# Optimization experiments

Measured on AMD Instinct MI355X. Metric: run time of the kernel, lower is better.

The kernel has to match this reference:

```python
import jax, jax.numpy as jnp
import numpy as np
import math

B, C, N, L = 32, 128, 2048, 1
H, DK, APT = 8, 16, 10
EPS = 1e-5


def conv1x1(x, W, b):
    # 1x1 Conv2d on [B, C, N, L]
    return jnp.einsum('oc,bcnl->bonl', W, x) + b[None, :, None, None]


def layer_norm_12(x):
    # normalize over dims (1, 2) as in the custom LayerNorm (no affine)
    mean = x.mean(axis=(1, 2), keepdims=True)
    var = x.var(axis=(1, 2), keepdims=True)
    return (x - mean) / jnp.sqrt(var + EPS)


def setup_inputs() -> dict:
    key = jax.random.key(0)
    ks = jax.random.split(key, 10)
    s = 0.05  # small-scale init for numerical stability
    inp = {
        'input': jax.random.normal(ks[0], (B, C, N, L), jnp.float32),
        'Wq': jax.random.normal(ks[1], (C, C), jnp.float32) * s,
        'bq': jnp.zeros((C,), jnp.float32),
        'Wv': jax.random.normal(ks[2], (C, C), jnp.float32) * s,
        'bv': jnp.zeros((C,), jnp.float32),
        'Wc': jax.random.normal(ks[3], (C, C), jnp.float32) * s,
        'bc': jnp.zeros((C,), jnp.float32),
        'memory': jax.random.normal(ks[4], (H, L, N, DK), jnp.float32) * s,
        'sa_weight': jnp.ones((C, N, L), jnp.float32),
        'sa_bias': jnp.zeros((C, N, L), jnp.float32),
        'nodevec1': jax.random.normal(ks[5], (N, APT), jnp.float32),
        'nodevec2': jax.random.normal(ks[6], (APT, N), jnp.float32),
        'Wg1': jax.random.normal(ks[7], (C, C), jnp.float32) * s,
        'bg1': jnp.zeros((C,), jnp.float32),
        'Wg2': jax.random.normal(ks[8], (C, C), jnp.float32) * s,
        'bg2': jnp.zeros((C,), jnp.float32),
        'Wg3': jax.random.normal(ks[9], (C, C), jnp.float32) * s,
        'bg3': jnp.zeros((C,), jnp.float32),
    }
    return inp


def reference(input, Wq, bq, Wv, bv, Wc, bc, memory, sa_weight, sa_bias,
              nodevec1, nodevec2, Wg1, bg1, Wg2, bg2, Wg3, bg3):
    scale = math.sqrt(DK)

    def split_heads(t):  # [B,C,N,L] -> [B,H,L,N,DK]
        return t.reshape(B, H, DK, N, L).transpose(0, 1, 4, 3, 2)

    # SpatialAttention (Conv = 1x1 conv + relu; dropout off in eval)
    q = jax.nn.relu(conv1x1(input, Wq, bq))
    v = jax.nn.relu(conv1x1(input, Wv, bv))
    query = jax.nn.softmax(split_heads(q) / scale, axis=-1)     # [B,H,L,N,DK]
    value = split_heads(v)                                       # [B,H,L,N,DK]
    key = jax.nn.softmax(memory / scale, axis=-1)                # [H,L,N,DK]
    Aapt = jax.nn.softmax(jax.nn.relu(nodevec1 @ nodevec2), axis=-1)  # [N,N]

    kv = jnp.einsum('hlnx,bhlny->bhlxy', key, value)             # [B,H,L,DK,DK]
    attn_qkv = jnp.einsum('bhlnx,bhlxy->bhlny', query, kv)       # [B,H,L,N,DK]
    attn_dyn = jnp.einsum('nm,bhlnc->bhlnc', Aapt, value)        # row-sum scaling
    x = attn_qkv + attn_dyn

    # merge heads back to [B,C,N,L] and apply concat conv (Conv = conv+relu)
    x = x.transpose(0, 1, 4, 3, 2).reshape(B, C, N, L)
    x = jax.nn.relu(conv1x1(x, Wc, bc))
    x = x * sa_weight[None] + sa_bias[None] + x                  # affine branch

    # Encoder wrap
    x = x + input
    x = layer_norm_12(x)
    g = conv1x1(x, Wg1, bg1) * jax.nn.sigmoid(conv1x1(x, Wg2, bg2))
    g = conv1x1(g, Wg3, bg3)                                     # GLU
    x = g + x
    x = x * sa_weight[None] + sa_bias[None] + x
    x = layer_norm_12(x)
    return x
```

## Files before the change

kernel.cpp:

```cpp
#include <hip/hip_runtime.h>
#include <hip/hip_bf16.h>
#include <math.h>

#define DI __device__ __forceinline__

typedef short bf16x8 __attribute__((ext_vector_type(8)));
typedef float f32x4 __attribute__((ext_vector_type(4)));

constexpr int BB = 32, CC = 128, NN = 2048;
constexpr float EPSf = 1e-5f;
constexpr float RCN = 1.0f / (CC * (float)NN);

#define MFMA(a,b,c) __builtin_amdgcn_mfma_f32_16x16x32_bf16(a,b,c,0,0,0)

DI unsigned short f2b(float f){
    union { __hip_bfloat16 h; unsigned short u; } v;
    v.h = __float2bfloat16(f);
    return v.u;
}
DI float b2f(unsigned short h){
    union { unsigned u; float f; } v; v.u = ((unsigned)h) << 16;
    return v.f;
}
DI float sigm(float x){ return 1.0f / (1.0f + __expf(-x)); }

__global__ __launch_bounds__(256) void k_prep(
    const float* __restrict__ Wq, const float* __restrict__ Wv,
    const float* __restrict__ Wc, const float* __restrict__ Wg1,
    const float* __restrict__ Wg2, const float* __restrict__ Wg3,
    const float* __restrict__ mem, const float* __restrict__ saw,
    const float* __restrict__ sab,
    unsigned short* __restrict__ Wb, float* __restrict__ rs,
    unsigned short* __restrict__ ksT, unsigned short* __restrict__ sawb,
    unsigned short* __restrict__ sabb)
{
    const int tid = threadIdx.x;
    if (blockIdx.x < 96) {
        const int i = blockIdx.x * 256 + tid;
        const int m = i >> 12, q = i & 4095;
        const float* src = (m==0)?Wq:(m==1)?Wv:(m==2)?Wc:(m==3)?Wg1:(m==4)?Wg2:Wg3;
        f32x4 w = *(const f32x4*)&src[q * 4];
        ushort4 p; p.x=f2b(w[0]); p.y=f2b(w[1]); p.z=f2b(w[2]); p.w=f2b(w[3]);
        *(ushort4*)&Wb[(size_t)m * 16384 + q * 4] = p;
    } else if (blockIdx.x == 96) {
        const float* src = (tid < 128) ? Wg1 : Wg2;
        const int o = tid & 127;
        float s = 0.f;
#pragma unroll
        for (int j = 0; j < 32; j++) {
            f32x4 a = *(const f32x4*)&src[o * 128 + j * 4];
            s += a[0] + a[1] + a[2] + a[3];
        }
        rs[tid] = s;
    } else if (blockIdx.x < 161) {
        const int row = (blockIdx.x - 97) * 256 + tid;
        const int h = row >> 11, n = row & 2047;
        const float* p = mem + (size_t)row * 16;
        float v[16];
        f32x4 t0 = *(const f32x4*)(p);
        f32x4 t1 = *(const f32x4*)(p + 4);
        f32x4 t2 = *(const f32x4*)(p + 8);
        f32x4 t3 = *(const f32x4*)(p + 12);
#pragma unroll
        for (int j = 0; j < 4; j++) { v[j]=t0[j]; v[4+j]=t1[j]; v[8+j]=t2[j]; v[12+j]=t3[j]; }
        float mx = v[0];
#pragma unroll
        for (int x = 1; x < 16; x++) mx = fmaxf(mx, v[x]);
        float s = 0.f;
#pragma unroll
        for (int x = 0; x < 16; x++) { v[x] = __expf((v[x] - mx) * 0.25f); s += v[x]; }
        const float is = 1.0f / s;
#pragma unroll
        for (int x = 0; x < 16; x++)
            ksT[((size_t)(h * 16 + x)) * NN + n] = f2b(v[x] * is);
    } else {
        const int i = (blockIdx.x - 161) * 256 + tid;
        const int m = i >> 16, q = i & 65535;
        const float* src = m ? sab : saw;
        unsigned short* dst = m ? sabb : sawb;
        f32x4 w = *(const f32x4*)&src[q * 4];
        ushort4 p; p.x=f2b(w[0]); p.y=f2b(w[1]); p.z=f2b(w[2]); p.w=f2b(w[3]);
        *(ushort4*)&dst[q * 4] = p;
    }
}

__global__ __launch_bounds__(256,1) void k_qv(
    const float* __restrict__ in, const unsigned short* __restrict__ WqB,
    const unsigned short* __restrict__ WvB, const float* __restrict__ bq,
    const float* __restrict__ bv, unsigned short* __restrict__ qT,
    unsigned short* __restrict__ vT, unsigned short* __restrict__ inT)
{
    __shared__ unsigned short tile[128 * 136];
    const int b = blockIdx.x >> 4, n0 = (blockIdx.x & 15) * 128;
    const int tid = threadIdx.x, l = tid & 63, wid = tid >> 6;
    const int wo = wid & 1, wn = wid >> 1, lr = l & 15, lg = l >> 4;
    f32x4 accq[4][4], accv[4][4];
    const f32x4 z = {0.f,0.f,0.f,0.f};
#pragma unroll
    for (int i = 0; i < 4; i++)
#pragma unroll
        for (int j = 0; j < 4; j++) { accq[i][j] = z; accv[i][j] = z; }
    const float* inb = in + (size_t)b * CC * NN;
#pragma unroll
    for (int ks = 0; ks < 4; ks++) {
        const int cb = ks * 32 + lg * 8;
        bf16x8 aq[4], av[4];
#pragma unroll
        for (int mf = 0; mf < 4; mf++) {
            const int o = wo*64 + mf*16 + lr;
            aq[mf] = *(const bf16x8*)&WqB[o * 128 + cb];
            av[mf] = *(const bf16x8*)&WvB[o * 128 + cb];
        }
        bf16x8 bx[4];
#pragma unroll
        for (int nf = 0; nf < 4; nf++) {
            const int n = n0 + wn*64 + nf*16 + lr;
            union { bf16x8 v; unsigned short u[8]; } t;
#pragma unroll
            for (int j = 0; j < 8; j++) t.u[j] = f2b(inb[(size_t)(cb + j) * NN + n]);
            bx[nf] = t.v;
        }
        if (wo == 0) {
#pragma unroll
            for (int nf = 0; nf < 4; nf++)
                *(bf16x8*)&tile[(wn*64 + nf*16 + lr) * 136 + cb] = bx[nf];
        }
#pragma unroll
        for (int mf = 0; mf < 4; mf++)
#pragma unroll
            for (int nf = 0; nf < 4; nf++) {
                accq[mf][nf] = MFMA(aq[mf], bx[nf], accq[mf][nf]);
                accv[mf][nf] = MFMA(av[mf], bx[nf], accv[mf][nf]);
            }
    }
    __syncthreads();
#pragma unroll
    for (int p = 0; p < 8; p++) {
        const int row = p*16 + (tid >> 4), col = (tid & 15) * 8;
        *(uint4*)&inT[((size_t)b * NN + n0 + row) * CC + col] =
            *(const uint4*)&tile[row * 136 + col];
    }
    __syncthreads();
#pragma unroll
    for (int mf = 0; mf < 4; mf++) {
        const int ob = wo*64 + mf*16 + lg*4;
        const f32x4 b4 = *(const f32x4*)&bq[ob];
#pragma unroll
        for (int nf = 0; nf < 4; nf++) {
            const int nl = wn*64 + nf*16 + lr;
            f32x4 a = accq[mf][nf];
            ushort4 pk;
            pk.x = f2b(fmaxf(a[0]+b4[0],0.f)); pk.y = f2b(fmaxf(a[1]+b4[1],0.f));
            pk.z = f2b(fmaxf(a[2]+b4[2],0.f)); pk.w = f2b(fmaxf(a[3]+b4[3],0.f));
            *(ushort4*)&tile[nl * 136 + ob] = pk;
        }
    }
    __syncthreads();
#pragma unroll
    for (int p = 0; p < 8; p++) {
        const int row = p*16 + (tid >> 4), col = (tid & 15) * 8;
        *(uint4*)&qT[((size_t)b * NN + n0 + row) * CC + col] =
            *(const uint4*)&tile[row * 136 + col];
    }
    __syncthreads();
#pragma unroll
    for (int mf = 0; mf < 4; mf++) {
        const int ob = wo*64 + mf*16 + lg*4;
        const f32x4 b4 = *(const f32x4*)&bv[ob];
#pragma unroll
        for (int nf = 0; nf < 4; nf++) {
            const int nl = wn*64 + nf*16 + lr;
            f32x4 a = accv[mf][nf];
            ushort4 pk;
            pk.x = f2b(fmaxf(a[0]+b4[0],0.f)); pk.y = f2b(fmaxf(a[1]+b4[1],0.f));
            pk.z = f2b(fmaxf(a[2]+b4[2],0.f)); pk.w = f2b(fmaxf(a[3]+b4[3],0.f));
            *(ushort4*)&tile[nl * 136 + ob] = pk;
        }
    }
    __syncthreads();
#pragma unroll
    for (int p = 0; p < 8; p++) {
        const int row = p*16 + (tid >> 4), col = (tid & 15) * 8;
        *(uint4*)&vT[((size_t)b * NN + n0 + row) * CC + col] =
            *(const uint4*)&tile[row * 136 + col];
    }
}

__global__ __launch_bounds__(256) void k_kv(const unsigned short* __restrict__ ksT,
                                            const unsigned short* __restrict__ vT,
                                            float* __restrict__ kvb)
{
    __shared__ unsigned short vt[4 * 16 * 520];
    __shared__ float red[1024];
    const int b = blockIdx.x >> 3, h = blockIdx.x & 7;
    const int tid = threadIdx.x, l = tid & 63, wid = tid >> 6;
    const int n0 = wid * 512;
    unsigned short* vtw = vt + wid * (16 * 520);
    const unsigned short* vb = vT + ((size_t)b * NN + n0) * CC + h * 16;
#pragma unroll
    for (int r = 0; r < 8; r++) {
        const int nl = r * 64 + l;
        uint4 q0 = *(const uint4*)&vb[(size_t)nl * CC];
        uint4 q1 = *(const uint4*)&vb[(size_t)nl * CC + 8];
        const unsigned uu[8] = {q0.x,q0.y,q0.z,q0.w,q1.x,q1.y,q1.z,q1.w};
#pragma unroll
        for (int k = 0; k < 8; k++) {
            vtw[(2*k)*520 + nl]   = (unsigned short)(uu[k] & 0xffffu);
            vtw[(2*k+1)*520 + nl] = (unsigned short)(uu[k] >> 16);
        }
    }
    const int lr = l & 15, lg = l >> 4;
    const unsigned short* ka = ksT + (size_t)h * 16 * NN;
    f32x4 acc = {0.f,0.f,0.f,0.f};
#pragma unroll
    for (int kk = 0; kk < 16; kk++) {
        bf16x8 af = *(const bf16x8*)&ka[(size_t)lr * NN + n0 + kk*32 + lg*8];
        bf16x8 bf = *(const bf16x8*)&vtw[lr * 520 + kk*32 + lg*8];
        acc = MFMA(af, bf, acc);
    }
#pragma unroll
    for (int r = 0; r < 4; r++)
        red[wid * 256 + (lg*4 + r) * 16 + lr] = acc[r];
    __syncthreads();
    {
        const float s = red[tid] + red[256 + tid] + red[512 + tid] + red[768 + tid];
        kvb[((size_t)(b * 8 + h)) * 256 + tid] = s;
    }
}

__global__ __launch_bounds__(256,2) void k_attnC(
    const unsigned short* __restrict__ qT, unsigned short* __restrict__ vT,
    const float* __restrict__ kvb, const unsigned short* __restrict__ WcB,
    const float* __restrict__ bc, const unsigned short* __restrict__ sawb,
    const unsigned short* __restrict__ sabb, const unsigned short* __restrict__ inT,
    float* __restrict__ part1)
{
    __shared__ float kvl[8 * 260];
    __shared__ unsigned short xc[128 * 136];
    __shared__ float red[8];
    const int b = blockIdx.x >> 4, n0 = (blockIdx.x & 15) * 128;
    const int tid = threadIdx.x;
    {
        const float* kp = kvb + (size_t)b * 2048 + (tid >> 5) * 256 + (tid & 31) * 8;
        f32x4 v0 = *(const f32x4*)kp;
        f32x4 v1 = *(const f32x4*)(kp + 4);
        float* dst = &kvl[(tid >> 5) * 260 + (tid & 31) * 8];
        *(f32x4*)dst = v0; *(f32x4*)(dst + 4) = v1;
    }
    __syncthreads();
#pragma unroll 1
    for (int it = 0; it < 4; it++) {
        const int idx = it * 256 + tid;
        const int nl = idx >> 3, h = idx & 7;
        const size_t base = ((size_t)b * NN + n0 + nl) * CC + h * 16;
        uint4 u0 = *(const uint4*)(qT + base);
        uint4 u1 = *(const uint4*)(qT + base + 8);
        uint4 w0 = *(const uint4*)(vT + base);
        uint4 w1 = *(const uint4*)(vT + base + 8);
        unsigned uu[8] = {u0.x,u0.y,u0.z,u0.w,u1.x,u1.y,u1.z,u1.w};
        float mx = -1e30f;
#pragma unroll
        for (int j = 0; j < 8; j++) {
            mx = fmaxf(mx, b2f((unsigned short)(uu[j] & 0xffffu)));
            mx = fmaxf(mx, b2f((unsigned short)(uu[j] >> 16)));
        }
        const float* kh = &kvl[h * 260];
        f32x4 r0 = {0,0,0,0}, r1 = {0,0,0,0}, r2 = {0,0,0,0}, r3 = {0,0,0,0};
        float s = 0.f;
#pragma unroll
        for (int x = 0; x < 16; x++) {
            const unsigned short qh = (x & 1) ? (unsigned short)(uu[x >> 1] >> 16)
                                              : (unsigned short)(uu[x >> 1] & 0xffffu);
            const float e = __expf((b2f(qh) - mx) * 0.25f);
            s += e;
            const f32x4 k0 = *(const f32x4*)&kh[x * 16];
            const f32x4 k1 = *(const f32x4*)&kh[x * 16 + 4];
            const f32x4 k2 = *(const f32x4*)&kh[x * 16 + 8];
            const f32x4 k3 = *(const f32x4*)&kh[x * 16 + 12];
#pragma unroll
            for (int j = 0; j < 4; j++) {
                r0[j] = fmaf(e, k0[j], r0[j]);
                r1[j] = fmaf(e, k1[j], r1[j]);
                r2[j] = fmaf(e, k2[j], r2[j]);
                r3[j] = fmaf(e, k3[j], r3[j]);
            }
        }
        const float is = 1.0f / s;
        unsigned vv[8] = {w0.x,w0.y,w0.z,w0.w,w1.x,w1.y,w1.z,w1.w};
        unsigned short* xp = &xc[nl * 136 + h * 16];
#pragma unroll
        for (int j2 = 0; j2 < 4; j2++) {
            const f32x4 rr = (j2==0)?r0:(j2==1)?r1:(j2==2)?r2:r3;
            ushort4 pk;
            pk.x = f2b(rr[0]*is + b2f((unsigned short)(vv[2*j2]   & 0xffffu)));
            pk.y = f2b(rr[1]*is + b2f((unsigned short)(vv[2*j2]   >> 16)));
            pk.z = f2b(rr[2]*is + b2f((unsigned short)(vv[2*j2+1] & 0xffffu)));
            pk.w = f2b(rr[3]*is + b2f((unsigned short)(vv[2*j2+1] >> 16)));
            *(ushort4*)&xp[j2 * 4] = pk;
        }
    }
    __syncthreads();
    const int l = tid & 63, wid = tid >> 6;
    const int wo = wid & 1, wn = wid >> 1, lr = l & 15, lg = l >> 4;
    f32x4 acc[4][4];
    const f32x4 z = {0.f,0.f,0.f,0.f};
#pragma unroll
    for (int i = 0; i < 4; i++)
#pragma unroll
        for (int j = 0; j < 4; j++) acc[i][j] = z;
#pragma unroll
    for (int ks = 0; ks < 4; ks++) {
        const int cb = ks * 32 + lg * 8;
        bf16x8 af[4];
#pragma unroll
        for (int mf = 0; mf < 4; mf++)
            af[mf] = *(const bf16x8*)&WcB[(wo*64 + mf*16 + lr) * 128 + cb];
        bf16x8 bx[4];
#pragma unroll
        for (int nf = 0; nf < 4; nf++)
            bx[nf] = *(const bf16x8*)&xc[(wn*64 + nf*16 + lr) * 136 + cb];
#pragma unroll
        for (int mf = 0; mf < 4; mf++)
#pragma unroll
            for (int nf = 0; nf < 4; nf++)
                acc[mf][nf] = MFMA(af[mf], bx[nf], acc[mf][nf]);
    }
    __syncthreads();
    float sum = 0.f, ssq = 0.f;
#pragma unroll
    for (int mf = 0; mf < 4; mf++) {
        const int ob = wo*64 + mf*16 + lg*4;
        const f32x4 b4 = *(const f32x4*)&bc[ob];
#pragma unroll
        for (int nf = 0; nf < 4; nf++) {
            const int nl = wn*64 + nf*16 + lr;
            const int n = n0 + nl;
            f32x4 a = acc[mf][nf];
            const ushort4 iu = *(const ushort4*)&inT[((size_t)b * NN + n) * CC + ob];
            float ys[4];
#pragma unroll
            for (int r = 0; r < 4; r++) {
                const int o = ob + r;
                const float t = fmaxf(a[r] + b4[r], 0.f);
                const float sw = b2f(sawb[(size_t)o * NN + n]);
                const float sb = b2f(sabb[(size_t)o * NN + n]);
                const unsigned short iv = (r==0)?iu.x:(r==1)?iu.y:(r==2)?iu.z:iu.w;
                float y = t * sw + sb + t + b2f(iv);
                sum += y; ssq += y * y;
                ys[r] = y;
            }
            ushort4 pk;
            pk.x = f2b(ys[0]); pk.y = f2b(ys[1]); pk.z = f2b(ys[2]); pk.w = f2b(ys[3]);
            *(ushort4*)&xc[nl * 136 + ob] = pk;
        }
        __builtin_amdgcn_sched_barrier(0);
    }
    __syncthreads();
#pragma unroll
    for (int p = 0; p < 8; p++) {
        const int row = p*16 + (tid >> 4), col = (tid & 15) * 8;
        *(uint4*)&vT[((size_t)b * NN + n0 + row) * CC + col] =
            *(const uint4*)&xc[row * 136 + col];
    }
#pragma unroll
    for (int off = 32; off > 0; off >>= 1) {
        sum += __shfl_down(sum, off);
        ssq += __shfl_down(ssq, off);
    }
    if ((tid & 63) == 0) { red[wid*2] = sum; red[wid*2+1] = ssq; }
    __syncthreads();
    if (tid == 0) {
        part1[2 * blockIdx.x]     = red[0]+red[2]+red[4]+red[6];
        part1[2 * blockIdx.x + 1] = red[1]+red[3]+red[5]+red[7];
    }
}

__global__ __launch_bounds__(256,1) void k_glu3(
    const unsigned short* __restrict__ y1,
    const unsigned short* __restrict__ W1B, const unsigned short* __restrict__ W2B,
    const unsigned short* __restrict__ W3B,
    const float* __restrict__ b1, const float* __restrict__ b2,
    const float* __restrict__ b3, const float* __restrict__ rs,
    const float* __restrict__ part1, const unsigned short* __restrict__ sawb,
    const unsigned short* __restrict__ sabb, unsigned short* __restrict__ X2,
    float* __restrict__ part2)
{
    __shared__ unsigned short yt[128 * 136];
    __shared__ unsigned short gx[128 * 136];
    __shared__ float cs[256];
    __shared__ float red[8];
    const int b = blockIdx.x >> 4, n0 = (blockIdx.x & 15) * 128;
    const int tid = threadIdx.x;
    float s0 = 0.f, q0 = 0.f;
#pragma unroll
    for (int t = 0; t < 16; t++) { s0 += part1[(b*16+t)*2]; q0 += part1[(b*16+t)*2+1]; }
    const float mean = s0 * RCN;
    const float var  = q0 * RCN - mean * mean;
    const float inv  = rsqrtf(var + EPSf);
    {
        const int cq = tid & 15;
#pragma unroll
        for (int it = 0; it < 8; it++) {
            const int n = it * 16 + (tid >> 4);
            uint4 u = *(const uint4*)&y1[((size_t)b * NN + n0 + n) * CC + cq * 8];
            *(uint4*)&yt[n * 136 + cq * 8] = u;
        }
    }
    {
        const int o = tid & 127;
        const float bb = (tid < 128) ? b1[o] : b2[o];
        cs[tid] = bb - mean * inv * rs[tid];
    }
    __syncthreads();
    const int l = tid & 63, wid = tid >> 6;
    const int wo = wid & 1, wn = wid >> 1, lr = l & 15, lg = l >> 4;
    {
        f32x4 acc1[4][4], acc2[4][4];
        const f32x4 z = {0.f,0.f,0.f,0.f};
#pragma unroll
        for (int i = 0; i < 4; i++)
#pragma unroll
            for (int j = 0; j < 4; j++) { acc1[i][j] = z; acc2[i][j] = z; }
#pragma unroll
        for (int ks = 0; ks < 4; ks++) {
            const int cb = ks * 32 + lg * 8;
            bf16x8 a1[4], a2[4];
#pragma unroll
            for (int mf = 0; mf < 4; mf++) {
                const int o = wo*64 + mf*16 + lr;
                a1[mf] = *(const bf16x8*)&W1B[o * 128 + cb];
                a2[mf] = *(const bf16x8*)&W2B[o * 128 + cb];
            }
            bf16x8 bx[4];
#pragma unroll
            for (int nf = 0; nf < 4; nf++)
                bx[nf] = *(const bf16x8*)&yt[(wn*64 + nf*16 + lr) * 136 + cb];
#pragma unroll
            for (int mf = 0; mf < 4; mf++)
#pragma unroll
                for (int nf = 0; nf < 4; nf++) {
                    acc1[mf][nf] = MFMA(a1[mf], bx[nf], acc1[mf][nf]);
                    acc2[mf][nf] = MFMA(a2[mf], bx[nf], acc2[mf][nf]);
                }
        }
#pragma unroll
        for (int mf = 0; mf < 4; mf++) {
            const int ob = wo*64 + mf*16 + lg*4;
            const f32x4 c1 = *(const f32x4*)&cs[ob];
            const f32x4 c2 = *(const f32x4*)&cs[128 + ob];
#pragma unroll
            for (int nf = 0; nf < 4; nf++) {
                const int nl = wn*64 + nf*16 + lr;
                ushort4 pk;
                float g1, g2;
                g1 = acc1[mf][nf][0]*inv + c1[0]; g2 = acc2[mf][nf][0]*inv + c2[0];
                pk.x = f2b(g1 * sigm(g2));
                g1 = acc1[mf][nf][1]*inv + c1[1]; g2 = acc2[mf][nf][1]*inv + c2[1];
                pk.y = f2b(g1 * sigm(g2));
                g1 = acc1[mf][nf][2]*inv + c1[2]; g2 = acc2[mf][nf][2]*inv + c2[2];
                pk.z = f2b(g1 * sigm(g2));
                g1 = acc1[mf][nf][3]*inv + c1[3]; g2 = acc2[mf][nf][3]*inv + c2[3];
                pk.w = f2b(g1 * sigm(g2));
                *(ushort4*)&gx[nl * 136 + ob] = pk;
            }
        }
    }
    __syncthreads();
    f32x4 acc[4][4];
    const f32x4 z = {0.f,0.f,0.f,0.f};
#pragma unroll
    for (int i = 0; i < 4; i++)
#pragma unroll
        for (int j = 0; j < 4; j++) acc[i][j] = z;
#pragma unroll
    for (int ks = 0; ks < 4; ks++) {
        const int cb = ks * 32 + lg * 8;
        bf16x8 af[4];
#pragma unroll
        for (int mf = 0; mf < 4; mf++)
            af[mf] = *(const bf16x8*)&W3B[(wo*64 + mf*16 + lr) * 128 + cb];
        bf16x8 bx[4];
#pragma unroll
        for (int nf = 0; nf < 4; nf++)
            bx[nf] = *(const bf16x8*)&gx[(wn*64 + nf*16 + lr) * 136 + cb];
#pragma unroll
        for (int mf = 0; mf < 4; mf++)
#pragma unroll
            for (int nf = 0; nf < 4; nf++)
                acc[mf][nf] = MFMA(af[mf], bx[nf], acc[mf][nf]);
    }
    __syncthreads();
    float sum = 0.f, ssq = 0.f;
#pragma unroll
    for (int mf = 0; mf < 4; mf++) {
        const int ob = wo*64 + mf*16 + lg*4;
        const f32x4 b4 = *(const f32x4*)&b3[ob];
#pragma unroll
        for (int nf = 0; nf < 4; nf++) {
            const int nl = wn*64 + nf*16 + lr;
            const int n = n0 + nl;
            ushort4 yq = *(const ushort4*)&yt[nl * 136 + ob];
            f32x4 a = acc[mf][nf];
            float ys[4];
#pragma unroll
            for (int r = 0; r < 4; r++) {
                const int o = ob + r;
                const unsigned short ev = (r==0)?yq.x:(r==1)?yq.y:(r==2)?yq.z:yq.w;
                const float t = a[r] + b4[r] + (b2f(ev) - mean) * inv;
                const float sw = b2f(sawb[(size_t)o * NN + n]);
                const float sb = b2f(sabb[(size_t)o * NN + n]);
                const float y = t * sw + sb + t;
                sum += y; ssq += y * y;
                ys[r] = y;
            }
            ushort4 pk;
            pk.x = f2b(ys[0]); pk.y = f2b(ys[1]); pk.z = f2b(ys[2]); pk.w = f2b(ys[3]);
            *(ushort4*)&gx[nl * 136 + ob] = pk;
        }
        __builtin_amdgcn_sched_barrier(0);
    }
    __syncthreads();
#pragma unroll
    for (int p = 0; p < 8; p++) {
        const int row = p*16 + (tid >> 4), col = (tid & 15) * 8;
        *(uint4*)&X2[((size_t)b * NN + n0 + row) * CC + col] =
            *(const uint4*)&gx[row * 136 + col];
    }
#pragma unroll
    for (int off = 32; off > 0; off >>= 1) {
        sum += __shfl_down(sum, off);
        ssq += __shfl_down(ssq, off);
    }
    if ((tid & 63) == 0) { red[wid*2] = sum; red[wid*2+1] = ssq; }
    __syncthreads();
    if (tid == 0) {
        part2[2 * blockIdx.x]     = red[0]+red[2]+red[4]+red[6];
        part2[2 * blockIdx.x + 1] = red[1]+red[3]+red[5]+red[7];
    }
}

__global__ __launch_bounds__(256) void k_lnfin(const unsigned short* __restrict__ x2,
                                               const float* __restrict__ part2,
                                               float* __restrict__ out)
{
    __shared__ unsigned ts[64 * 69];
    const int b = blockIdx.x >> 5, n0 = (blockIdx.x & 31) * 64;
    const int tid = threadIdx.x;
    float s0 = 0.f, q0 = 0.f;
#pragma unroll
    for (int t = 0; t < 16; t++) { s0 += part2[(b*16+t)*2]; q0 += part2[(b*16+t)*2+1]; }
    const float mean = s0 * RCN;
    const float var  = q0 * RCN - mean * mean;
    const float inv  = rsqrtf(var + EPSf);
    {
        const int n = tid >> 2, qd = tid & 3;
        const unsigned short* src = x2 + ((size_t)b * NN + n0 + n) * CC + qd * 32;
        uint4 a0 = *(const uint4*)(src);
        uint4 a1 = *(const uint4*)(src + 8);
        uint4 a2 = *(const uint4*)(src + 16);
        uint4 a3 = *(const uint4*)(src + 24);
        unsigned u[16] = {a0.x,a0.y,a0.z,a0.w, a1.x,a1.y,a1.z,a1.w,
                          a2.x,a2.y,a2.z,a2.w, a3.x,a3.y,a3.z,a3.w};
#pragma unroll
        for (int k = 0; k < 16; k++)
            ts[(qd * 16 + k) * 69 + n] = u[k];
    }
    __syncthreads();
#pragma unroll
    for (int pass = 0; pass < 8; pass++) {
        const int c = pass * 16 + (tid >> 4), nq = tid & 15;
        const int cp = c >> 1, hi = c & 1;
        f32x4 v;
#pragma unroll
        for (int j = 0; j < 4; j++) {
            const unsigned u = ts[cp * 69 + nq * 4 + j];
            const unsigned short hv = hi ? (unsigned short)(u >> 16)
                                         : (unsigned short)(u & 0xffffu);
            v[j] = (b2f(hv) - mean) * inv;
        }
        *(f32x4*)&out[((size_t)b * CC + c) * NN + n0 + nq * 4] = v;
    }
}

extern "C" void kernel_launch(void* const* d_in, const int* in_sizes, int n_in,
                              void* d_out, int out_size, void* d_ws, size_t ws_size,
                              hipStream_t stream)
{
    const float* input = (const float*)d_in[0];
    const float* Wq  = (const float*)d_in[1];
    const float* bq  = (const float*)d_in[2];
    const float* Wv  = (const float*)d_in[3];
    const float* bv  = (const float*)d_in[4];
    const float* Wc  = (const float*)d_in[5];
    const float* bc  = (const float*)d_in[6];
    const float* mem = (const float*)d_in[7];
    const float* saw = (const float*)d_in[8];
    const float* sab = (const float*)d_in[9];
    const float* Wg1 = (const float*)d_in[12];
    const float* bg1 = (const float*)d_in[13];
    const float* Wg2 = (const float*)d_in[14];
    const float* bg2 = (const float*)d_in[15];
    const float* Wg3 = (const float*)d_in[16];
    const float* bg3 = (const float*)d_in[17];
    float* out = (float*)d_out;

    unsigned char* wsb = (unsigned char*)d_ws;
    unsigned short* qT  = (unsigned short*)(wsb);
    unsigned short* vT  = (unsigned short*)(wsb + 16777216);
    unsigned short* ksT = (unsigned short*)(wsb + 33554432);
    float* kvb   = (float*)(wsb + 34078720);
    unsigned short* Wb  = (unsigned short*)(wsb + 34340864);
    float* rs    = (float*)(wsb + 34537472);
    float* part1 = (float*)(wsb + 34538496);
    float* part2 = (float*)(wsb + 34542592);
    unsigned short* inT  = (unsigned short*)d_out;
    unsigned short* sawb = (unsigned short*)((unsigned char*)d_out + 16777216);
    unsigned short* sabb = sawb + 262144;

    k_prep <<<673,  256, 0, stream>>>(Wq, Wv, Wc, Wg1, Wg2, Wg3, mem, saw, sab,
                                      Wb, rs, ksT, sawb, sabb);
    k_qv   <<<512,  256, 0, stream>>>(input, Wb, Wb + 16384, bq, bv, qT, vT, inT);
    k_kv   <<<256,  256, 0, stream>>>(ksT, vT, kvb);
    k_attnC<<<512,  256, 0, stream>>>(qT, vT, kvb, Wb + 2*16384, bc, sawb, sabb,
                                      inT, part1);
    k_glu3 <<<512,  256, 0, stream>>>(vT, Wb + 3*16384, Wb + 4*16384, Wb + 5*16384,
                                      bg1, bg2, bg3, rs, part1, sawb, sabb, qT, part2);
    k_lnfin<<<1024, 256, 0, stream>>>(qT, part2, out);
}
```

Baseline: 124.9 us.

## Move Q projection into attention kernel and split dual GEMMs to raise occupancy

Measured after the change: 119.7 us. -4.1%, faster.

```diff
diff --git a/kernel.cpp b/kernel.cpp
--- a/kernel.cpp
+++ b/kernel.cpp
@@ -84,33 +84,29 @@
     }
 }
 
-__global__ __launch_bounds__(256,1) void k_qv(
-    const float* __restrict__ in, const unsigned short* __restrict__ WqB,
-    const unsigned short* __restrict__ WvB, const float* __restrict__ bq,
-    const float* __restrict__ bv, unsigned short* __restrict__ qT,
-    unsigned short* __restrict__ vT, unsigned short* __restrict__ inT)
+__global__ __launch_bounds__(256,2) void k_v(
+    const float* __restrict__ in, const unsigned short* __restrict__ WvB,
+    const float* __restrict__ bv, unsigned short* __restrict__ vT,
+    unsigned short* __restrict__ inT)
 {
     __shared__ unsigned short tile[128 * 136];
     const int b = blockIdx.x >> 4, n0 = (blockIdx.x & 15) * 128;
     const int tid = threadIdx.x, l = tid & 63, wid = tid >> 6;
     const int wo = wid & 1, wn = wid >> 1, lr = l & 15, lg = l >> 4;
-    f32x4 accq[4][4], accv[4][4];
+    f32x4 acc[4][4];
     const f32x4 z = {0.f,0.f,0.f,0.f};
 #pragma unroll
     for (int i = 0; i < 4; i++)
 #pragma unroll
-        for (int j = 0; j < 4; j++) { accq[i][j] = z; accv[i][j] = z; }
+        for (int j = 0; j < 4; j++) acc[i][j] = z;
     const float* inb = in + (size_t)b * CC * NN;
 #pragma unroll
     for (int ks = 0; ks < 4; ks++) {
         const int cb = ks * 32 + lg * 8;
-        bf16x8 aq[4], av[4];
-#pragma unroll
-        for (int mf = 0; mf < 4; mf++) {
-            const int o = wo*64 + mf*16 + lr;
-            aq[mf] = *(const bf16x8*)&WqB[o * 128 + cb];
-            av[mf] = *(const bf16x8*)&WvB[o * 128 + cb];
-        }
+        bf16x8 av[4];
+#pragma unroll
+        for (int mf = 0; mf < 4; mf++)
+            av[mf] = *(const bf16x8*)&WvB[(wo*64 + mf*16 + lr) * 128 + cb];
         bf16x8 bx[4];
 #pragma unroll
         for (int nf = 0; nf < 4; nf++) {
@@ -128,10 +124,8 @@
 #pragma unroll
         for (int mf = 0; mf < 4; mf++)
 #pragma unroll
-            for (int nf = 0; nf < 4; nf++) {
-                accq[mf][nf] = MFMA(aq[mf], bx[nf], accq[mf][nf]);
-                accv[mf][nf] = MFMA(av[mf], bx[nf], accv[mf][nf]);
-            }
+            for (int nf = 0; nf < 4; nf++)
+                acc[mf][nf] = MFMA(av[mf], bx[nf], acc[mf][nf]);
     }
     __syncthreads();
 #pragma unroll
@@ -144,33 +138,11 @@
 #pragma unroll
     for (int mf = 0; mf < 4; mf++) {
         const int ob = wo*64 + mf*16 + lg*4;
-        const f32x4 b4 = *(const f32x4*)&bq[ob];
+        const f32x4 b4 = *(const f32x4*)&bv[ob];
 #pragma unroll
         for (int nf = 0; nf < 4; nf++) {
             const int nl = wn*64 + nf*16 + lr;
-            f32x4 a = accq[mf][nf];
-            ushort4 pk;
-            pk.x = f2b(fmaxf(a[0]+b4[0],0.f)); pk.y = f2b(fmaxf(a[1]+b4[1],0.f));
-            pk.z = f2b(fmaxf(a[2]+b4[2],0.f)); pk.w = f2b(fmaxf(a[3]+b4[3],0.f));
-            *(ushort4*)&tile[nl * 136 + ob] = pk;
-        }
-    }
-    __syncthreads();
-#pragma unroll
-    for (int p = 0; p < 8; p++) {
-        const int row = p*16 + (tid >> 4), col = (tid & 15) * 8;
-        *(uint4*)&qT[((size_t)b * NN + n0 + row) * CC + col] =
-            *(const uint4*)&tile[row * 136 + col];
-    }
-    __syncthreads();
-#pragma unroll
-    for (int mf = 0; mf < 4; mf++) {
-        const int ob = wo*64 + mf*16 + lg*4;
-        const f32x4 b4 = *(const f32x4*)&bv[ob];
-#pragma unroll
-        for (int nf = 0; nf < 4; nf++) {
-            const int nl = wn*64 + nf*16 + lr;
-            f32x4 a = accv[mf][nf];
+            f32x4 a = acc[mf][nf];
             ushort4 pk;
             pk.x = f2b(fmaxf(a[0]+b4[0],0.f)); pk.y = f2b(fmaxf(a[1]+b4[1],0.f));
             pk.z = f2b(fmaxf(a[2]+b4[2],0.f)); pk.w = f2b(fmaxf(a[3]+b4[3],0.f));
@@ -229,14 +201,15 @@
 }
 
 __global__ __launch_bounds__(256,2) void k_attnC(
-    const unsigned short* __restrict__ qT, unsigned short* __restrict__ vT,
-    const float* __restrict__ kvb, const unsigned short* __restrict__ WcB,
-    const float* __restrict__ bc, const unsigned short* __restrict__ sawb,
-    const unsigned short* __restrict__ sabb, const unsigned short* __restrict__ inT,
+    const unsigned short* __restrict__ inT, unsigned short* __restrict__ vT,
+    const float* __restrict__ kvb,
+    const unsigned short* __restrict__ WqB, const float* __restrict__ bq,
+    const unsigned short* __restrict__ WcB, const float* __restrict__ bc,
+    const unsigned short* __restrict__ sawb, const unsigned short* __restrict__ sabb,
     float* __restrict__ part1)
 {
     __shared__ float kvl[8 * 260];
-    __shared__ unsigned short xc[128 * 136];
+    __shared__ unsigned short xq[128 * 136];
     __shared__ float red[8];
     const int b = blockIdx.x >> 4, n0 = (blockIdx.x & 15) * 128;
     const int tid = threadIdx.x;
@@ -247,16 +220,59 @@
         float* dst = &kvl[(tid >> 5) * 260 + (tid & 31) * 8];
         *(f32x4*)dst = v0; *(f32x4*)(dst + 4) = v1;
     }
+    const int l = tid & 63, wid = tid >> 6;
+    const int wo = wid & 1, wn = wid >> 1, lr = l & 15, lg = l >> 4;
+    {
+        f32x4 acc[4][4];
+        const f32x4 z = {0.f,0.f,0.f,0.f};
+#pragma unroll
+        for (int i = 0; i < 4; i++)
+#pragma unroll
+            for (int j = 0; j < 4; j++) acc[i][j] = z;
+        const unsigned short* ab = inT + (size_t)b * NN * CC;
+#pragma unroll
+        for (int ks = 0; ks < 4; ks++) {
+            const int cb = ks * 32 + lg * 8;
+            bf16x8 af[4];
+#pragma unroll
+            for (int mf = 0; mf < 4; mf++)
+                af[mf] = *(const bf16x8*)&WqB[(wo*64 + mf*16 + lr) * 128 + cb];
+            bf16x8 bx[4];
+#pragma unroll
+            for (int nf = 0; nf < 4; nf++)
+                bx[nf] = *(const bf16x8*)&ab[(size_t)(n0 + wn*64 + nf*16 + lr) * CC + cb];
+#pragma unroll
+            for (int mf = 0; mf < 4; mf++)
+#pragma unroll
+                for (int nf = 0; nf < 4; nf++)
+                    acc[mf][nf] = MFMA(af[mf], bx[nf], acc[mf][nf]);
+        }
+#pragma unroll
+        for (int mf = 0; mf < 4; mf++) {
+            const int ob = wo*64 + mf*16 + lg*4;
+            const f32x4 b4 = *(const f32x4*)&bq[ob];
+#pragma unroll
+            for (int nf = 0; nf < 4; nf++) {
+                const int nl = wn*64 + nf*16 + lr;
+                f32x4 a = acc[mf][nf];
+                ushort4 pk;
+                pk.x = f2b(fmaxf(a[0]+b4[0],0.f)); pk.y = f2b(fmaxf(a[1]+b4[1],0.f));
+                pk.z = f2b(fmaxf(a[2]+b4[2],0.f)); pk.w = f2b(fmaxf(a[3]+b4[3],0.f));
+                *(ushort4*)&xq[nl * 136 + ob] = pk;
+            }
+        }
+    }
     __syncthreads();
 #pragma unroll 1
     for (int it = 0; it < 4; it++) {
         const int idx = it * 256 + tid;
         const int nl = idx >> 3, h = idx & 7;
         const size_t base = ((size_t)b * NN + n0 + nl) * CC + h * 16;
-        uint4 u0 = *(const uint4*)(qT + base);
-        uint4 u1 = *(const uint4*)(qT + base + 8);
         uint4 w0 = *(const uint4*)(vT + base);
         uint4 w1 = *(const uint4*)(vT + base + 8);
+        const unsigned short* qp = &xq[nl * 136 + h * 16];
+        uint4 u0 = *(const uint4*)qp;
+        uint4 u1 = *(const uint4*)(qp + 8);
         unsigned uu[8] = {u0.x,u0.y,u0.z,u0.w,u1.x,u1.y,u1.z,u1.w};
         float mx = -1e30f;
 #pragma unroll
@@ -287,7 +303,7 @@
         }
         const float is = 1.0f / s;
         unsigned vv[8] = {w0.x,w0.y,w0.z,w0.w,w1.x,w1.y,w1.z,w1.w};
-        unsigned short* xp = &xc[nl * 136 + h * 16];
+        unsigned short* xp = &xq[nl * 136 + h * 16];
 #pragma unroll
         for (int j2 = 0; j2 < 4; j2++) {
             const f32x4 rr = (j2==0)?r0:(j2==1)?r1:(j2==2)?r2:r3;
@@ -300,8 +316,6 @@
         }
     }
     __syncthreads();
-    const int l = tid & 63, wid = tid >> 6;
-    const int wo = wid & 1, wn = wid >> 1, lr = l & 15, lg = l >> 4;
     f32x4 acc[4][4];
     const f32x4 z = {0.f,0.f,0.f,0.f};
 #pragma unroll
@@ -318,7 +332,7 @@
         bf16x8 bx[4];
 #pragma unroll
         for (int nf = 0; nf < 4; nf++)
-            bx[nf] = *(const bf16x8*)&xc[(wn*64 + nf*16 + lr) * 136 + cb];
+            bx[nf] = *(const bf16x8*)&xq[(wn*64 + nf*16 + lr) * 136 + cb];
 #pragma unroll
         for (int mf = 0; mf < 4; mf++)
 #pragma unroll
@@ -351,16 +365,15 @@
             }
             ushort4 pk;
             pk.x = f2b(ys[0]); pk.y = f2b(ys[1]); pk.z = f2b(ys[2]); pk.w = f2b(ys[3]);
-            *(ushort4*)&xc[nl * 136 + ob] = pk;
-        }
-        __builtin_amdgcn_sched_barrier(0);
+            *(ushort4*)&xq[nl * 136 + ob] = pk;
+        }
     }
     __syncthreads();
 #pragma unroll
     for (int p = 0; p < 8; p++) {
         const int row = p*16 + (tid >> 4), col = (tid & 15) * 8;
         *(uint4*)&vT[((size_t)b * NN + n0 + row) * CC + col] =
-            *(const uint4*)&xc[row * 136 + col];
+            *(const uint4*)&xq[row * 136 + col];
     }
 #pragma unroll
     for (int off = 32; off > 0; off >>= 1) {
@@ -375,7 +388,7 @@
     }
 }
 
-__global__ __launch_bounds__(256,1) void k_glu3(
+__global__ __launch_bounds__(256,2) void k_glu3(
     const unsigned short* __restrict__ y1,
     const unsigned short* __restrict__ W1B, const unsigned short* __restrict__ W2B,
     const unsigned short* __restrict__ W3B,
@@ -414,23 +427,20 @@
     __syncthreads();
     const int l = tid & 63, wid = tid >> 6;
     const int wo = wid & 1, wn = wid >> 1, lr = l & 15, lg = l >> 4;
-    {
-        f32x4 acc1[4][4], acc2[4][4];
-        const f32x4 z = {0.f,0.f,0.f,0.f};
+    const f32x4 z = {0.f,0.f,0.f,0.f};
+    {
+        f32x4 acc[4][4];
 #pragma unroll
         for (int i = 0; i < 4; i++)
 #pragma unroll
-            for (int j = 0; j < 4; j++) { acc1[i][j] = z; acc2[i][j] = z; }
+            for (int j = 0; j < 4; j++) acc[i][j] = z;
 #pragma unroll
         for (int ks = 0; ks < 4; ks++) {
             const int cb = ks * 32 + lg * 8;
-            bf16x8 a1[4], a2[4];
-#pragma unroll
-            for (int mf = 0; mf < 4; mf++) {
-                const int o = wo*64 + mf*16 + lr;
-                a1[mf] = *(const bf16x8*)&W1B[o * 128 + cb];
-                a2[mf] = *(const bf16x8*)&W2B[o * 128 + cb];
-            }
+            bf16x8 af[4];
+#pragma unroll
+            for (int mf = 0; mf < 4; mf++)
+                af[mf] = *(const bf16x8*)&W1B[(wo*64 + mf*16 + lr) * 128 + cb];
             bf16x8 bx[4];
 #pragma unroll
             for (int nf = 0; nf < 4; nf++)
@@ -438,36 +448,67 @@
 #pragma unroll
             for (int mf = 0; mf < 4; mf++)
 #pragma unroll
-                for (int nf = 0; nf < 4; nf++) {
-                    acc1[mf][nf] = MFMA(a1[mf], bx[nf], acc1[mf][nf]);
-                    acc2[mf][nf] = MFMA(a2[mf], bx[nf], acc2[mf][nf]);
-                }
+                for (int nf = 0; nf < 4; nf++)
+                    acc[mf][nf] = MFMA(af[mf], bx[nf], acc[mf][nf]);
         }
 #pragma unroll
         for (int mf = 0; mf < 4; mf++) {
             const int ob = wo*64 + mf*16 + lg*4;
             const f32x4 c1 = *(const f32x4*)&cs[ob];
-            const f32x4 c2 = *(const f32x4*)&cs[128 + ob];
 #pragma unroll
             for (int nf = 0; nf < 4; nf++) {
                 const int nl = wn*64 + nf*16 + lr;
+                f32x4 a = acc[mf][nf];
                 ushort4 pk;
-                float g1, g2;
-                g1 = acc1[mf][nf][0]*inv + c1[0]; g2 = acc2[mf][nf][0]*inv + c2[0];
-                pk.x = f2b(g1 * sigm(g2));
-                g1 = acc1[mf][nf][1]*inv + c1[1]; g2 = acc2[mf][nf][1]*inv + c2[1];
-                pk.y = f2b(g1 * sigm(g2));
-                g1 = acc1[mf][nf][2]*inv + c1[2]; g2 = acc2[mf][nf][2]*inv + c2[2];
-                pk.z = f2b(g1 * sigm(g2));
-                g1 = acc1[mf][nf][3]*inv + c1[3]; g2 = acc2[mf][nf][3]*inv + c2[3];
-                pk.w = f2b(g1 * sigm(g2));
+                pk.x = f2b(a[0]*inv + c1[0]); pk.y = f2b(a[1]*inv + c1[1]);
+                pk.z = f2b(a[2]*inv + c1[2]); pk.w = f2b(a[3]*inv + c1[3]);
                 *(ushort4*)&gx[nl * 136 + ob] = pk;
             }
         }
     }
+    {
+        f32x4 acc[4][4];
+#pragma unroll
+        for (int i = 0; i < 4; i++)
+#pragma unroll
+            for (int j = 0; j < 4; j++) acc[i][j] = z;
+#pragma unroll
+        for (int ks = 0; ks < 4; ks++) {
+            const int cb = ks * 32 + lg * 8;
+            bf16x8 af[4];
+#pragma unroll
+            for (int mf = 0; mf < 4; mf++)
+                af[mf] = *(const bf16x8*)&W2B[(wo*64 + mf*16 + lr) * 128 + cb];
+            bf16x8 bx[4];
+#pragma unroll
+            for (int nf = 0; nf < 4; nf++)
+                bx[nf] = *(const bf16x8*)&yt[(wn*64 + nf*16 + lr) * 136 + cb];
+#pragma unroll
+            for (int mf = 0; mf < 4; mf++)
+#pragma unroll
+                for (int nf = 0; nf < 4; nf++)
+                    acc[mf][nf] = MFMA(af[mf], bx[nf], acc[mf][nf]);
+        }
+#pragma unroll
+        for (int mf = 0; mf < 4; mf++) {
+            const int ob = wo*64 + mf*16 + lg*4;
+            const f32x4 c2 = *(const f32x4*)&cs[128 + ob];
+#pragma unroll
+            for (int nf = 0; nf < 4; nf++) {
+                const int nl = wn*64 + nf*16 + lr;
+                f32x4 a = acc[mf][nf];
+                ushort4 g1 = *(const ushort4*)&gx[nl * 136 + ob];
+                ushort4 pk;
+                pk.x = f2b(b2f(g1.x) * sigm(a[0]*inv + c2[0]));
+                pk.y = f2b(b2f(g1.y) * sigm(a[1]*inv + c2[1]));
+                pk.z = f2b(b2f(g1.z) * sigm(a[2]*inv + c2[2]));
+                pk.w = f2b(b2f(g1.w) * sigm(a[3]*inv + c2[3]));
+                *(ushort4*)&gx[nl * 136 + ob] = pk;
+            }
+        }
+    }
     __syncthreads();
     f32x4 acc[4][4];
-    const f32x4 z = {0.f,0.f,0.f,0.f};
 #pragma unroll
     for (int i = 0; i < 4; i++)
 #pragma unroll
@@ -517,7 +558,6 @@
             pk.x = f2b(ys[0]); pk.y = f2b(ys[1]); pk.z = f2b(ys[2]); pk.w = f2b(ys[3]);
             *(ushort4*)&gx[nl * 136 + ob] = pk;
         }
-        __builtin_amdgcn_sched_barrier(0);
     }
     __syncthreads();
 #pragma unroll
@@ -605,7 +645,7 @@
     float* out = (float*)d_out;
 
     unsigned char* wsb = (unsigned char*)d_ws;
-    unsigned short* qT  = (unsigned short*)(wsb);
+    unsigned short* inT = (unsigned short*)(wsb);
     unsigned short* vT  = (unsigned short*)(wsb + 16777216);
     unsigned short* ksT = (unsigned short*)(wsb + 33554432);
     float* kvb   = (float*)(wsb + 34078720);
@@ -613,17 +653,16 @@
     float* rs    = (float*)(wsb + 34537472);
     float* part1 = (float*)(wsb + 34538496);
     float* part2 = (float*)(wsb + 34542592);
-    unsigned short* inT  = (unsigned short*)d_out;
-    unsigned short* sawb = (unsigned short*)((unsigned char*)d_out + 16777216);
+    unsigned short* sawb = (unsigned short*)d_out;
     unsigned short* sabb = sawb + 262144;
 
     k_prep <<<673,  256, 0, stream>>>(Wq, Wv, Wc, Wg1, Wg2, Wg3, mem, saw, sab,
                                       Wb, rs, ksT, sawb, sabb);
-    k_qv   <<<512,  256, 0, stream>>>(input, Wb, Wb + 16384, bq, bv, qT, vT, inT);
+    k_v    <<<512,  256, 0, stream>>>(input, Wb + 16384, bv, vT, inT);
     k_kv   <<<256,  256, 0, stream>>>(ksT, vT, kvb);
-    k_attnC<<<512,  256, 0, stream>>>(qT, vT, kvb, Wb + 2*16384, bc, sawb, sabb,
-                                      inT, part1);
+    k_attnC<<<512,  256, 0, stream>>>(inT, vT, kvb, Wb, bq, Wb + 2*16384, bc,
+                                      sawb, sabb, part1);
     k_glu3 <<<512,  256, 0, stream>>>(vT, Wb + 3*16384, Wb + 4*16384, Wb + 5*16384,
-                                      bg1, bg2, bg3, rs, part1, sawb, sabb, qT, part2);
-    k_lnfin<<<1024, 256, 0, stream>>>(qT, part2, out);
-}
+                                      bg1, bg2, bg3, rs, part1, sawb, sabb, inT, part2);
+    k_lnfin<<<1024, 256, 0, stream>>>(inT, part2, out);
+}
```
